# Kernel tuning notes

Measured on AMD Instinct MI355X. Metric: run time of the kernel, lower is better.

The kernel has to match this reference:

```python
import jax, jax.numpy as jnp
import numpy as np

FEATURE_SCALE = 0.25  # cfg.feature_scale
G = 4                 # deformable/offset groups
K = 3                 # deform kernel size
KK = K * K
PAD = 1


def conv2d(x, w, b=None):
    y = jax.lax.conv_general_dilated(x, w, (1, 1), ((PAD, PAD), (PAD, PAD)),
                                     dimension_numbers=('NCHW', 'OIHW', 'NCHW'))
    return y if b is None else y + b[None, :, None, None]


def bilinear_upsample_ac(x, fs):
    # F.interpolate(mode='bilinear', align_corners=True, scale_factor=fs)
    b, c, H, W = x.shape
    Ho, Wo = H * fs, W * fs
    sy = jnp.arange(Ho, dtype=x.dtype) * ((H - 1) / (Ho - 1))
    sx = jnp.arange(Wo, dtype=x.dtype) * ((W - 1) / (Wo - 1))
    y0 = jnp.clip(jnp.floor(sy).astype(jnp.int32), 0, H - 2)
    x0 = jnp.clip(jnp.floor(sx).astype(jnp.int32), 0, W - 2)
    wy = (sy - y0)[None, None, :, None]
    wx = (sx - x0)[None, None, None, :]
    rows = x[:, :, y0, :] * (1 - wy) + x[:, :, y0 + 1, :] * wy
    return rows[:, :, :, x0] * (1 - wx) + rows[:, :, :, x0 + 1] * wx


def deform_conv(x, offset, mask, w):
    # torchvision.ops.deform_conv2d, stride 1, pad 1, weight groups = 1,
    # offset/mask groups = G. offset layout: (b, G*KK*2, H, W), (dy, dx) pairs.
    b, C, H, W = x.shape
    Cg = C // G
    off = offset.reshape(b, G, KK, 2, H, W)
    ii = (jnp.arange(KK) // K).reshape(1, 1, KK, 1, 1).astype(x.dtype)
    jj = (jnp.arange(KK) % K).reshape(1, 1, KK, 1, 1).astype(x.dtype)
    ys = jnp.arange(H, dtype=x.dtype).reshape(1, 1, 1, H, 1)
    xs = jnp.arange(W, dtype=x.dtype).reshape(1, 1, 1, 1, W)
    py = ys - PAD + ii + off[:, :, :, 0]   # (b,G,KK,H,W)
    px = xs - PAD + jj + off[:, :, :, 1]
    xt = x.reshape(b, G, Cg, H, W).transpose(0, 1, 3, 4, 2)  # (b,G,H,W,Cg)
    y0f = jnp.floor(py)
    x0f = jnp.floor(px)
    wy = py - y0f
    wx = px - x0f
    y0 = y0f.astype(jnp.int32)
    x0 = x0f.astype(jnp.int32)
    bi = jnp.arange(b).reshape(b, 1, 1, 1, 1)
    gi = jnp.arange(G).reshape(1, G, 1, 1, 1)

    def corner(yi, xi, wgt):
        valid = ((yi >= 0) & (yi < H) & (xi >= 0) & (xi < W)).astype(x.dtype)
        v = xt[bi, gi, jnp.clip(yi, 0, H - 1), jnp.clip(xi, 0, W - 1)]  # (b,G,KK,H,W,Cg)
        return v * (wgt * valid)[..., None]

    s = (corner(y0, x0, (1 - wy) * (1 - wx)) + corner(y0, x0 + 1, (1 - wy) * wx)
         + corner(y0 + 1, x0, wy * (1 - wx)) + corner(y0 + 1, x0 + 1, wy * wx))
    s = s * mask.reshape(b, G, KK, H, W)[..., None]
    wr = w.reshape(w.shape[0], G, Cg, KK)
    return jnp.einsum('bgkhwc,ogck->bohw', s, wr)


def _align(sou_list, ref_list, params):
    cat_feat, offset_vs = [], []
    for i in (3, 2, 1):
        sou, ref = sou_list[i - 1], ref_list[i - 1]
        b, C, H, W = sou.shape
        Cg = C // G
        off_w, off_b, mod_w, mod_b, reg_w = params[i]
        off_in = jnp.concatenate([sou.reshape(b, G, Cg, H, W),
                                  ref.reshape(b, G, Cg, H, W)], axis=2)
        off_in = off_in.reshape(b * G, 2 * Cg, H, W)
        offset = conv2d(off_in, off_w, off_b).reshape(b, G * 2 * KK, H, W)
        rng = min(H, W) * 0.5 / 2
        offset_map = rng * 2 * jax.nn.sigmoid(offset) - rng
        modulator = 2.0 * jax.nn.sigmoid(conv2d(sou, mod_w, mod_b))
        feat = deform_conv(sou, offset_map, modulator, reg_w)
        fs = int(1 // (FEATURE_SCALE / 2 ** (i - 1)))
        oy = jnp.mean(offset_map[:, 0::2], axis=1, keepdims=True)
        ox = jnp.mean(offset_map[:, 1::2], axis=1, keepdims=True)
        ov = bilinear_upsample_ac(jnp.concatenate([oy, ox], axis=1), fs) * fs
        cat_feat.append(feat)
        offset_vs.append(ov)
    return tuple(cat_feat) + tuple(offset_vs)


def setup_inputs() -> dict:
    key = jax.random.key(0)
    ks = jax.random.split(key, 32)
    d = {}
    shapes = {1: (2, 64, 128, 128), 2: (2, 64, 64, 64), 3: (2, 64, 32, 32)}
    k = 0
    for i in (1, 2, 3):
        d[f'sou{i}'] = jax.random.normal(ks[k], shapes[i], jnp.float32); k += 1
        d[f'ref{i}'] = jax.random.normal(ks[k], shapes[i], jnp.float32); k += 1
    Cg = 64 // G
    for i in (1, 2, 3):
        d[f'off_w{i}'] = jax.random.normal(ks[k], (2 * KK, 2 * Cg, K, K), jnp.float32) * 0.05; k += 1
        d[f'off_b{i}'] = jax.random.normal(ks[k], (2 * KK,), jnp.float32) * 0.05; k += 1
        d[f'mod_w{i}'] = jax.random.normal(ks[k], (G * KK, 64, K, K), jnp.float32) * 0.05; k += 1
        d[f'mod_b{i}'] = jax.random.normal(ks[k], (G * KK,), jnp.float32) * 0.05; k += 1
        d[f'reg_w{i}'] = jax.random.normal(ks[k], (64, 64, K, K), jnp.float32) * 0.05; k += 1
    return d


def reference(sou1, sou2, sou3, ref1, ref2, ref3,
              off_w1, off_b1, mod_w1, mod_b1, reg_w1,
              off_w2, off_b2, mod_w2, mod_b2, reg_w2,
              off_w3, off_b3, mod_w3, mod_b3, reg_w3):
    params = {1: (off_w1, off_b1, mod_w1, mod_b1, reg_w1),
              2: (off_w2, off_b2, mod_w2, mod_b2, reg_w2),
              3: (off_w3, off_b3, mod_w3, mod_b3, reg_w3)}
    return _align([sou1, sou2, sou3], [ref1, ref2, ref3], params)
```

## Files before the change

### kernel.cpp

```cpp
#include <hip/hip_runtime.h>

typedef __attribute__((ext_vector_type(8))) short short8;
typedef __attribute__((ext_vector_type(4))) float f32x4;

__device__ __forceinline__ float sigmoidf_(float x) { return 1.f / (1.f + __expf(-x)); }
__device__ __forceinline__ unsigned bf16rne(float x) {
    unsigned b = __float_as_uint(x);
    return (b + 0x7FFFu + ((b >> 16) & 1u)) >> 16;
}


struct P {
    const float *sou0, *sou1, *sou2;
    const float *ref0, *ref1, *ref2;
    const float *ob0, *ob1, *ob2;
    const float *mb0, *mb1, *mb2;
    float* out;
    float* ws;
};

union U {
    uint4 u4; int4 i4; short8 s8; f32x4 f4;
};

__global__ __launch_bounds__(256) void repack_all(
    const float* __restrict__ ow0, const float* __restrict__ mw0, const float* __restrict__ rw0,
    const float* __restrict__ ow1, const float* __restrict__ mw1, const float* __restrict__ rw1,
    const float* __restrict__ ow2, const float* __restrict__ mw2, const float* __restrict__ rw2,
    float* __restrict__ dst) {
    const int lvl = blockIdx.y;
    const float* ow = lvl == 0 ? ow0 : (lvl == 1 ? ow1 : ow2);
    const float* mw = lvl == 0 ? mw0 : (lvl == 1 ? mw1 : mw2);
    const float* rw = lvl == 0 ? rw0 : (lvl == 1 ? rw1 : rw2);
    unsigned* d = (unsigned*)(dst + lvl * 62784);
    int i = blockIdx.x * 256 + threadIdx.x;
    if (i < 18432) {
        int jw = i & 3;
        int lane = (i >> 2) & 63;
        int t3 = i >> 8;
        int ks = t3 % 18, wvu = t3 / 18;
        int o = wvu * 16 + (lane & 15);
        int c0 = ks * 32 + (lane >> 4) * 8 + 2 * jw;
        int g0 = c0 / 144, r0 = c0 % 144;
        int c1 = c0 + 1;
        int g1 = c1 / 144, r1 = c1 % 144;
        float w0 = rw[o * 576 + (g0 * 16 + (r0 & 15)) * 9 + (r0 >> 4)];
        float w1 = rw[o * 576 + (g1 * 16 + (r1 & 15)) * 9 + (r1 >> 4)];
        d[i] = bf16rne(w0) | (bf16rne(w1) << 16);
    } else if (i < 23040) {
        int o2 = i - 18432;
        int jw = o2 & 3;
        int lane = (o2 >> 2) & 63;
        int t2 = o2 >> 8;
        int tap = t2 >> 1, nt = t2 & 1;
        int n = nt * 16 + (lane & 15);
        int ic0 = (lane >> 4) * 8 + 2 * jw;
        float w0 = (n < 18) ? ow[n * 288 + ic0 * 9 + tap] : 0.f;
        float w1 = (n < 18) ? ow[n * 288 + (ic0 + 1) * 9 + tap] : 0.f;
        d[36864 + o2] = bf16rne(w0) | (bf16rne(w1) << 16);
    } else if (i < 36864) {
        int o3 = i - 23040;
        int jw = o3 & 3;
        int lane = (o3 >> 2) & 63;
        int t3 = o3 >> 8;
        int nt = t3 % 3, tc = t3 / 3;
        int tap = tc >> 1, c = tc & 1;
        int n = nt * 16 + (lane & 15);
        int ic0 = c * 32 + (lane >> 4) * 8 + 2 * jw;
        float w0 = (n < 36) ? mw[n * 576 + ic0 * 9 + tap] : 0.f;
        float w1 = (n < 36) ? mw[n * 576 + (ic0 + 1) * 9 + tap] : 0.f;
        d[41472 + o3] = bf16rne(w0) | (bf16rne(w1) << 16);
    }
}

__global__ __launch_bounds__(256) void k1_prep(P p) {
    __shared__ __align__(16) char smem[28512];
    const int t = blockIdx.x;
    float* ws = p.ws;
    const int tid = threadIdx.x;

    if (t < 2688) {
        int lvl, j;
        if (t < 2048) { lvl = 0; j = t; }
        else if (t < 2560) { lvl = 1; j = t - 2048; }
        else { lvl = 2; j = t - 2560; }
        const int logW = 7 - lvl;
        const int W = 1 << logW, H = W, HW = H * W;
        const int nper = 256 >> (2 * lvl);
        const int qb = j % nper, g = (j / nper) & 3, b = j / (nper * 4);
        const int q0 = qb * 64;
        const int hlo = q0 >> logW;
        const int xlo = q0 & (W - 1);
        const int cols = (W >= 64) ? 66 : 34;
        const int rcTot = (W >= 64) ? 198 : 136;
        const float* sou = lvl == 0 ? p.sou0 : (lvl == 1 ? p.sou1 : p.sou2);
        const float* ref = lvl == 0 ? p.ref0 : (lvl == 1 ? p.ref1 : p.ref2);
        const float* bases = sou + (size_t)(b * 64 + g * 16) * HW;
        const float* baser = ref + (size_t)(b * 64 + g * 16) * HW;
        unsigned* ldsW = (unsigned*)smem;
        const bool sact = tid < rcTot;
        const int srow = tid / cols, scol = tid - srow * cols;
        const int grow = hlo - 1 + srow, gcol = xlo - 1 + scol;
        const bool inb = sact && grow >= 0 && grow < H && gcol >= 0 && gcol < W;
        const size_t goff = inb ? ((size_t)grow * W + gcol) : 0;
#pragma unroll
        for (int c8 = 0; c8 < 4; ++c8) {
            const float* p0 = (c8 < 2) ? bases + (size_t)(c8 * 8) * HW
                                       : baser + (size_t)((c8 - 2) * 8) * HW;
            float v[8];
#pragma unroll
            for (int jj = 0; jj < 8; ++jj) v[jj] = inb ? p0[(size_t)jj * HW + goff] : 0.f;
            if (sact) {
                uint4 wv;
                wv.x = bf16rne(v[0]) | (bf16rne(v[1]) << 16);
                wv.y = bf16rne(v[2]) | (bf16rne(v[3]) << 16);
                wv.z = bf16rne(v[4]) | (bf16rne(v[5]) << 16);
                wv.w = bf16rne(v[6]) | (bf16rne(v[7]) << 16);
                *(uint4*)&ldsW[tid * 20 + c8 * 4] = wv;
            }
        }
        __syncthreads();
        const int wvu = __builtin_amdgcn_readfirstlane(tid >> 6);
        const int lane = tid & 63, quad = lane >> 4, lo16 = lane & 15;
        const int qg = q0 + wvu * 16 + lo16;
        const int rowB = (qg >> logW) - hlo;
        const int colB = (qg & (W - 1)) - xlo;
        const unsigned short* ldsS = (const unsigned short*)smem;
        const unsigned* WBO = (const unsigned*)(ws + 4730880 + lvl * 62784) + 36864;
        f32x4 acc[2];
        acc[0] = (f32x4){0.f, 0.f, 0.f, 0.f};
        acc[1] = (f32x4){0.f, 0.f, 0.f, 0.f};
#pragma unroll
        for (int tap = 0; tap < 9; ++tap) {
            const int ky = tap / 3, kx = tap - ky * 3;
            const int rc = (rowB + ky) * cols + colB + kx;
            U au; au.s8 = *(const short8*)&ldsS[rc * 40 + quad * 8];
#pragma unroll
            for (int nt = 0; nt < 2; ++nt) {
                U bu; bu.u4 = *(const uint4*)(WBO + ((tap * 2 + nt) * 64 + lane) * 4);
                acc[nt] = __builtin_amdgcn_mfma_f32_16x16x32_bf16(au.s8, bu.s8, acc[nt], 0, 0, 0);
            }
        }
        const float* bias = lvl == 0 ? p.ob0 : (lvl == 1 ? p.ob1 : p.ob2);
        float* OFFM = ws + (lvl == 0 ? 0 : (lvl == 1 ? 2359296 : 2949120));
        const float rng = 0.25f * (float)H;
#pragma unroll
        for (int nt = 0; nt < 2; ++nt) {
            const int o = nt * 16 + lo16;
            if (o < 18) {
                const float bb = bias[o];
                float* op = OFFM + (size_t)(b * 72 + g * 18 + o) * HW + q0 + wvu * 16 + quad * 4;
#pragma unroll
                for (int rg = 0; rg < 4; ++rg)
                    op[rg] = rng * (2.f * sigmoidf_(acc[nt][rg] + bb) - 1.f);
            }
        }
    } else {
        const int i1 = t - 2688;
        int lvl, j;
        if (i1 < 512) { lvl = 0; j = i1; }
        else if (i1 < 640) { lvl = 1; j = i1 - 512; }
        else { lvl = 2; j = i1 - 640; }
        const int logW = 7 - lvl;
        const int W = 1 << logW, H = W, HW = H * W;
        const int nper = 256 >> (2 * lvl);
        const int qb = j % nper, b = j / nper;
        const int q0 = qb * 64;
        const int hlo = q0 >> logW;
        const int xlo = q0 & (W - 1);
        const int cols = (W >= 64) ? 66 : 34;
        const int rcTot = (W >= 64) ? 198 : 136;
        const float* sou = lvl == 0 ? p.sou0 : (lvl == 1 ? p.sou1 : p.sou2);
        const float* base = sou + (size_t)b * 64 * HW;
        unsigned* ldsW = (unsigned*)smem;
        const bool sact = tid < rcTot;
        const int srow = tid / cols, scol = tid - srow * cols;
        const int grow = hlo - 1 + srow, gcol = xlo - 1 + scol;
        const bool inb = sact && grow >= 0 && grow < H && gcol >= 0 && gcol < W;
        const size_t goff = inb ? ((size_t)grow * W + gcol) : 0;
#pragma unroll
        for (int c8 = 0; c8 < 8; ++c8) {
            const float* p0 = base + (size_t)(c8 * 8) * HW;
            float v[8];
#pragma unroll
            for (int jj = 0; jj < 8; ++jj) v[jj] = inb ? p0[(size_t)jj * HW + goff] : 0.f;
            if (sact) {
                uint4 wv;
                wv.x = bf16rne(v[0]) | (bf16rne(v[1]) << 16);
                wv.y = bf16rne(v[2]) | (bf16rne(v[3]) << 16);
                wv.z = bf16rne(v[4]) | (bf16rne(v[5]) << 16);
                wv.w = bf16rne(v[6]) | (bf16rne(v[7]) << 16);
                *(uint4*)&ldsW[tid * 36 + c8 * 4] = wv;
            }
        }
        __syncthreads();
        unsigned* XTb = (unsigned*)(ws + 4919232) +
                        (lvl == 0 ? 0 : (lvl == 1 ? 1048576 : 1310720));
#pragma unroll
        for (int u = 0; u < 2; ++u) {
            const int idx = tid * 2 + u;
            const int px = idx >> 3, gh = idx & 7;
            const int g = gh >> 1, half = gh & 1;
            const int rc = ((px >> logW) + 1) * cols + (px & (W - 1)) + 1;
            uint4 v = *(const uint4*)&ldsW[rc * 36 + g * 8 + half * 4];
            *(uint4*)(XTb + ((size_t)(b * 4 + g) * HW + q0 + px) * 8 + half * 4) = v;
        }
        const int wvu = __builtin_amdgcn_readfirstlane(tid >> 6);
        const int lane = tid & 63, quad = lane >> 4, lo16 = lane & 15;
        const int qg = q0 + wvu * 16 + lo16;
        const int rowB = (qg >> logW) - hlo;
        const int colB = (qg & (W - 1)) - xlo;
        const unsigned short* ldsS = (const unsigned short*)smem;
        const unsigned* WBM = (const unsigned*)(ws + 4730880 + lvl * 62784) + 41472;
        f32x4 acc[3];
        acc[0] = (f32x4){0.f, 0.f, 0.f, 0.f};
        acc[1] = (f32x4){0.f, 0.f, 0.f, 0.f};
        acc[2] = (f32x4){0.f, 0.f, 0.f, 0.f};
#pragma unroll
        for (int tap = 0; tap < 9; ++tap) {
            const int ky = tap / 3, kx = tap - ky * 3;
            const int rc = (rowB + ky) * cols + colB + kx;
#pragma unroll
            for (int c = 0; c < 2; ++c) {
                U au; au.s8 = *(const short8*)&ldsS[rc * 72 + c * 32 + quad * 8];
#pragma unroll
                for (int nt = 0; nt < 3; ++nt) {
                    U bu;
                    bu.u4 = *(const uint4*)(WBM + (((tap * 2 + c) * 3 + nt) * 64 + lane) * 4);
                    acc[nt] = __builtin_amdgcn_mfma_f32_16x16x32_bf16(au.s8, bu.s8, acc[nt], 0, 0, 0);
                }
            }
        }
        const float* bias = lvl == 0 ? p.mb0 : (lvl == 1 ? p.mb1 : p.mb2);
        float* MOD = ws + (lvl == 0 ? 3096576 : (lvl == 1 ? 4276224 : 4571136));
#pragma unroll
        for (int nt = 0; nt < 3; ++nt) {
            const int o = nt * 16 + lo16;
            if (o < 36) {
                const float bb = bias[o];
                float* op = MOD + (size_t)(b * 36 + o) * HW + q0 + wvu * 16 + quad * 4;
#pragma unroll
                for (int rg = 0; rg < 4; ++rg)
                    op[rg] = 2.f * sigmoidf_(acc[nt][rg] + bb);
            }
        }
    }
}

__global__ __launch_bounds__(256) void k2_fused(P p) {
    __shared__ unsigned lds[96 * 33];
    const int t = blockIdx.x;
    float* ws = p.ws;
    const int tid = threadIdx.x;
    if (t < 1344) {
        int lvl, j;
        if (t < 1024) { lvl = 0; j = t; }
        else if (t < 1280) { lvl = 1; j = t - 1024; }
        else { lvl = 2; j = t - 1280; }
        const int logW = 7 - lvl;
        const int W = 1 << logW, H = W, HW = H * W;
        const int nper = 512 >> (2 * lvl);
        const int qb = j % nper, b = j / nper;
        const int q0 = qb * 32;
        const float* OFFM = ws + (lvl == 0 ? 0 : (lvl == 1 ? 2359296 : 2949120));
        const float* MOD = ws + (lvl == 0 ? 3096576 : (lvl == 1 ? 4276224 : 4571136));
        const unsigned* XTb = (const unsigned*)(ws + 4919232) +
                              (lvl == 0 ? 0 : (lvl == 1 ? 1048576 : 1310720));
        const unsigned* WB = (const unsigned*)(ws + 4730880 + lvl * 62784);
        float* outp = p.out + (lvl == 0 ? 655360 : (lvl == 1 ? 131072 : 0));
        const int wvu = __builtin_amdgcn_readfirstlane(tid >> 6);
        const int lane = tid & 63, quad = lane >> 4, lo16 = lane & 15;
        f32x4 acc[2];
        acc[0] = (f32x4){0.f, 0.f, 0.f, 0.f};
        acc[1] = (f32x4){0.f, 0.f, 0.f, 0.f};
        for (int c = 0; c < 3; ++c) {
            if (c) __syncthreads();
#pragma unroll
            for (int it = 0; it < 2; ++it) {
                const int task = it * 256 + tid;
                if (task < 384) {
                    const int gkl = task >> 5, px = task & 31;
                    const int gk = c * 12 + gkl;
                    const int g = gk / 9, k = gk - g * 9;
                    const int q = q0 + px;
                    const int h = q >> logW, xp = q & (W - 1);
                    const int ky = k / 3, kx = k - ky * 3;
                    float dy = OFFM[(size_t)(b * 72 + g * 18 + 2 * k) * HW + q];
                    float dx = OFFM[(size_t)(b * 72 + g * 18 + 2 * k + 1) * HW + q];
                    float m = MOD[(size_t)(b * 36 + g * 9 + k) * HW + q];
                    float py = (float)(h - 1 + ky) + dy;
                    float pxx = (float)(xp - 1 + kx) + dx;
                    float y0f = floorf(py), x0f = floorf(pxx);
                    float wy = py - y0f, wx = pxx - x0f;
                    int y0 = (int)y0f, x0 = (int)x0f;
                    const unsigned* xg = XTb + (size_t)(b * 4 + g) * HW * 8;
                    float s[16];
#pragma unroll
                    for (int cc = 0; cc < 16; ++cc) s[cc] = 0.f;
#pragma unroll
                    for (int cor = 0; cor < 4; ++cor) {
                        int yy = y0 + (cor >> 1), xx = x0 + (cor & 1);
                        float cw = ((cor >> 1) ? wy : 1.f - wy) * ((cor & 1) ? wx : 1.f - wx);
                        cw = (yy >= 0 && yy < H && xx >= 0 && xx < W) ? cw * m : 0.f;
                        int yc = min(max(yy, 0), H - 1), xc = min(max(xx, 0), W - 1);
                        const uint4* cp = (const uint4*)(xg + (size_t)((yc << logW) + xc) * 8);
                        unsigned cbuf[8];
                        *(uint4*)&cbuf[0] = cp[0];
                        *(uint4*)&cbuf[4] = cp[1];
#pragma unroll
                        for (int pr = 0; pr < 8; ++pr) {
                            float lo = __uint_as_float(cbuf[pr] << 16);
                            float hi = __uint_as_float(cbuf[pr] & 0xFFFF0000u);
                            s[2 * pr] = fmaf(cw, lo, s[2 * pr]);
                            s[2 * pr + 1] = fmaf(cw, hi, s[2 * pr + 1]);
                        }
                    }
#pragma unroll
                    for (int pr = 0; pr < 8; ++pr)
                        lds[(gkl * 8 + pr) * 33 + px] =
                            bf16rne(s[2 * pr]) | (bf16rne(s[2 * pr + 1]) << 16);
                }
            }
            __syncthreads();
            uint4 bfr[6];
#pragma unroll
            for (int k6 = 0; k6 < 6; ++k6)
                bfr[k6] = *(const uint4*)(WB + (((wvu * 18 + c * 6 + k6) * 64 + lane) << 2));
#pragma unroll
            for (int k6 = 0; k6 < 6; ++k6) {
                const int rb = k6 * 16 + quad * 4;
                U bu; bu.u4 = bfr[k6];
#pragma unroll
                for (int mt = 0; mt < 2; ++mt) {
                    const int px = mt * 16 + lo16;
                    U au;
                    au.i4.x = (int)lds[(rb + 0) * 33 + px];
                    au.i4.y = (int)lds[(rb + 1) * 33 + px];
                    au.i4.z = (int)lds[(rb + 2) * 33 + px];
                    au.i4.w = (int)lds[(rb + 3) * 33 + px];
                    acc[mt] = __builtin_amdgcn_mfma_f32_16x16x32_bf16(au.s8, bu.s8, acc[mt], 0, 0, 0);
                }
            }
        }
        float* op = outp + (size_t)(b * 64 + wvu * 16 + lo16) * HW + q0;
#pragma unroll
        for (int mt = 0; mt < 2; ++mt)
#pragma unroll
            for (int rg = 0; rg < 4; ++rg)
                op[mt * 16 + quad * 4 + rg] = acc[mt][rg];
    } else {
        int i = t - 1344;
        int lvl, j;
        if (i < 128) { lvl = 0; j = i; }
        else if (i < 160) { lvl = 1; j = i - 128; }
        else { lvl = 2; j = i - 160; }
        const int HW = 16384 >> (2 * lvl);
        const int nper = 64 >> (2 * lvl);
        const int qb = j % nper, b = j / nper;
        const float* OFFM = ws + (lvl == 0 ? 0 : (lvl == 1 ? 2359296 : 2949120));
        float* MEAN = ws + (lvl == 0 ? 4644864 : (lvl == 1 ? 4710400 : 4726784));
        const int q = qb * 256 + tid;
        const float* pp = OFFM + (size_t)b * 72 * HW + q;
        float sy = 0.f, sx = 0.f;
#pragma unroll
        for (int u = 0; u < 36; ++u) {
            sy += pp[(size_t)(2 * u) * HW];
            sx += pp[(size_t)(2 * u + 1) * HW];
        }
        MEAN[(size_t)(b * 2) * HW + q] = sy * (1.f / 36.f);
        MEAN[(size_t)(b * 2 + 1) * HW + q] = sx * (1.f / 36.f);
    }
}

__global__ __launch_bounds__(256) void k3_up(P p) {
    float* ws = p.ws;
    int flat = ((int)blockIdx.x * 256 + (int)threadIdx.x) * 4;
    int lvl = flat >> 20;
    int r = flat & 1048575;
    int b = r >> 19, c = (r >> 18) & 1;
    int pix = r & 262143;
    int yo = pix >> 9, xo = pix & 511;
    const int H = 128 >> lvl, W = H;
    const float* MEAN = ws + (lvl == 0 ? 4644864 : (lvl == 1 ? 4710400 : 4726784));
    const float* m = MEAN + (size_t)(b * 2 + c) * H * W;
    float* o = p.out + (lvl == 0 ? 4849664 : (lvl == 1 ? 3801088 : 2752512)) +
               ((size_t)(b * 2 + c) * 512 + yo) * 512 + xo;
    const float fs = (float)(4 << lvl);
    const float sc = (float)(H - 1) * (1.f / 511.f);
    float sy = yo * sc;
    int y0 = min((int)sy, H - 2);
    float wy = sy - (float)y0;
    float rr[4];
#pragma unroll
    for (int u = 0; u < 4; ++u) {
        float sx = (float)(xo + u) * sc;
        int x0 = min((int)sx, W - 2);
        float wx = sx - (float)x0;
        float v00 = m[y0 * W + x0], v01 = m[y0 * W + x0 + 1];
        float v10 = m[(y0 + 1) * W + x0], v11 = m[(y0 + 1) * W + x0 + 1];
        float r0 = v00 * (1.f - wy) + v10 * wy;
        float r1 = v01 * (1.f - wy) + v11 * wy;
        rr[u] = (r0 * (1.f - wx) + r1 * wx) * fs;
    }
    *(float4*)o = make_float4(rr[0], rr[1], rr[2], rr[3]);
}

extern "C" void kernel_launch(void* const* d_in, const int* in_sizes, int n_in,
                              void* d_out, int out_size, void* d_ws, size_t ws_size,
                              hipStream_t stream) {
    const float* fin[21];
    for (int i = 0; i < 21; ++i) fin[i] = (const float*)d_in[i];
    P p;
    if (in_sizes[1] == in_sizes[0]) {
        p.sou0 = fin[0]; p.ref0 = fin[1];
        p.sou1 = fin[2]; p.ref1 = fin[3];
        p.sou2 = fin[4]; p.ref2 = fin[5];
    } else {
        p.sou0 = fin[0]; p.sou1 = fin[1]; p.sou2 = fin[2];
        p.ref0 = fin[3]; p.ref1 = fin[4]; p.ref2 = fin[5];
    }
    p.ob0 = fin[7]; p.mb0 = fin[9];
    p.ob1 = fin[12]; p.mb1 = fin[14];
    p.ob2 = fin[17]; p.mb2 = fin[19];
    p.out = (float*)d_out;
    p.ws = (float*)d_ws;

    repack_all<<<dim3(144, 3), 256, 0, stream>>>(
        fin[6], fin[8], fin[10], fin[11], fin[13], fin[15], fin[16], fin[18], fin[20],
        p.ws + 4730880);
    k1_prep<<<dim3(3360), 256, 0, stream>>>(p);
    k2_fused<<<dim3(1512), 256, 0, stream>>>(p);
    k3_up<<<dim3(3072), 256, 0, stream>>>(p);
}
```

Measured before the change: 185.0 us.

## Merge offset and modulation conv blocks so one block loads each source tile once

Merges the separate offset-conv blocks (one per group) and modulation-conv blocks into a single block per spatial tile. The block stages all 64 source channels in LDS once and runs both convolutions from it, then reloads the reference channels into the same buffer. The offset conv's K dimension is repacked to tap-major 16-channel chunks (5 k-steps, zero-padded) so it can use the 72-wide LDS layout. This cuts repeated global reads of the sou/ref inputs and the grid from 3360 to 672 blocks. In exchange each block holds more accumulators and does longer serial work, and the padded K adds some wasted MFMA work.

After: 180.3 us. 2.5% less time.

```diff
diff --git a/kernel.cpp b/kernel.cpp
--- a/kernel.cpp
+++ b/kernel.cpp
@@ -47,19 +47,23 @@
         float w0 = rw[o * 576 + (g0 * 16 + (r0 & 15)) * 9 + (r0 >> 4)];
         float w1 = rw[o * 576 + (g1 * 16 + (r1 & 15)) * 9 + (r1 >> 4)];
         d[i] = bf16rne(w0) | (bf16rne(w1) << 16);
-    } else if (i < 23040) {
+    } else if (i < 23552) {
         int o2 = i - 18432;
         int jw = o2 & 3;
         int lane = (o2 >> 2) & 63;
         int t2 = o2 >> 8;
-        int tap = t2 >> 1, nt = t2 & 1;
+        int nt = t2 & 1;
+        int hk = t2 >> 1;
+        int ks = hk % 5, h = hk / 5;
         int n = nt * 16 + (lane & 15);
-        int ic0 = (lane >> 4) * 8 + 2 * jw;
-        float w0 = (n < 18) ? ow[n * 288 + ic0 * 9 + tap] : 0.f;
-        float w1 = (n < 18) ? ow[n * 288 + (ic0 + 1) * 9 + tap] : 0.f;
+        int K = ks * 32 + (lane >> 4) * 8 + 2 * jw;
+        int tap = K >> 4, ch = K & 15;
+        bool ok = (n < 18) && (tap < 9);
+        float w0 = ok ? ow[n * 288 + (h * 16 + ch) * 9 + tap] : 0.f;
+        float w1 = ok ? ow[n * 288 + (h * 16 + ch + 1) * 9 + tap] : 0.f;
         d[36864 + o2] = bf16rne(w0) | (bf16rne(w1) << 16);
-    } else if (i < 36864) {
-        int o3 = i - 23040;
+    } else if (i < 37376) {
+        int o3 = i - 23552;
         int jw = o3 & 3;
         int lane = (o3 >> 2) & 63;
         int t3 = o3 >> 8;
@@ -69,7 +73,7 @@
         int ic0 = c * 32 + (lane >> 4) * 8 + 2 * jw;
         float w0 = (n < 36) ? mw[n * 576 + ic0 * 9 + tap] : 0.f;
         float w1 = (n < 36) ? mw[n * 576 + (ic0 + 1) * 9 + tap] : 0.f;
-        d[41472 + o3] = bf16rne(w0) | (bf16rne(w1) << 16);
+        d[41984 + o3] = bf16rne(w0) | (bf16rne(w1) << 16);
     }
 }
 
@@ -79,158 +83,151 @@
     float* ws = p.ws;
     const int tid = threadIdx.x;
 
-    if (t < 2688) {
-        int lvl, j;
-        if (t < 2048) { lvl = 0; j = t; }
-        else if (t < 2560) { lvl = 1; j = t - 2048; }
-        else { lvl = 2; j = t - 2560; }
-        const int logW = 7 - lvl;
-        const int W = 1 << logW, H = W, HW = H * W;
-        const int nper = 256 >> (2 * lvl);
-        const int qb = j % nper, g = (j / nper) & 3, b = j / (nper * 4);
-        const int q0 = qb * 64;
-        const int hlo = q0 >> logW;
-        const int xlo = q0 & (W - 1);
-        const int cols = (W >= 64) ? 66 : 34;
-        const int rcTot = (W >= 64) ? 198 : 136;
-        const float* sou = lvl == 0 ? p.sou0 : (lvl == 1 ? p.sou1 : p.sou2);
-        const float* ref = lvl == 0 ? p.ref0 : (lvl == 1 ? p.ref1 : p.ref2);
-        const float* bases = sou + (size_t)(b * 64 + g * 16) * HW;
-        const float* baser = ref + (size_t)(b * 64 + g * 16) * HW;
-        unsigned* ldsW = (unsigned*)smem;
-        const bool sact = tid < rcTot;
-        const int srow = tid / cols, scol = tid - srow * cols;
-        const int grow = hlo - 1 + srow, gcol = xlo - 1 + scol;
-        const bool inb = sact && grow >= 0 && grow < H && gcol >= 0 && gcol < W;
-        const size_t goff = inb ? ((size_t)grow * W + gcol) : 0;
-#pragma unroll
-        for (int c8 = 0; c8 < 4; ++c8) {
-            const float* p0 = (c8 < 2) ? bases + (size_t)(c8 * 8) * HW
-                                       : baser + (size_t)((c8 - 2) * 8) * HW;
-            float v[8];
-#pragma unroll
-            for (int jj = 0; jj < 8; ++jj) v[jj] = inb ? p0[(size_t)jj * HW + goff] : 0.f;
-            if (sact) {
-                uint4 wv;
-                wv.x = bf16rne(v[0]) | (bf16rne(v[1]) << 16);
-                wv.y = bf16rne(v[2]) | (bf16rne(v[3]) << 16);
-                wv.z = bf16rne(v[4]) | (bf16rne(v[5]) << 16);
-                wv.w = bf16rne(v[6]) | (bf16rne(v[7]) << 16);
-                *(uint4*)&ldsW[tid * 20 + c8 * 4] = wv;
-            }
-        }
-        __syncthreads();
-        const int wvu = __builtin_amdgcn_readfirstlane(tid >> 6);
-        const int lane = tid & 63, quad = lane >> 4, lo16 = lane & 15;
-        const int qg = q0 + wvu * 16 + lo16;
-        const int rowB = (qg >> logW) - hlo;
-        const int colB = (qg & (W - 1)) - xlo;
-        const unsigned short* ldsS = (const unsigned short*)smem;
-        const unsigned* WBO = (const unsigned*)(ws + 4730880 + lvl * 62784) + 36864;
-        f32x4 acc[2];
-        acc[0] = (f32x4){0.f, 0.f, 0.f, 0.f};
-        acc[1] = (f32x4){0.f, 0.f, 0.f, 0.f};
-#pragma unroll
-        for (int tap = 0; tap < 9; ++tap) {
-            const int ky = tap / 3, kx = tap - ky * 3;
-            const int rc = (rowB + ky) * cols + colB + kx;
-            U au; au.s8 = *(const short8*)&ldsS[rc * 40 + quad * 8];
+    int lvl, j;
+    if (t < 512) { lvl = 0; j = t; }
+    else if (t < 640) { lvl = 1; j = t - 512; }
+    else { lvl = 2; j = t - 640; }
+    const int logW = 7 - lvl;
+    const int W = 1 << logW, H = W, HW = H * W;
+    const int nper = 256 >> (2 * lvl);
+    const int qb = j % nper, b = j / nper;
+    const int q0 = qb * 64;
+    const int hlo = q0 >> logW;
+    const int xlo = q0 & (W - 1);
+    const int cols = (W >= 64) ? 66 : 34;
+    const int rcTot = (W >= 64) ? 198 : 136;
+    const float* sou = lvl == 0 ? p.sou0 : (lvl == 1 ? p.sou1 : p.sou2);
+    const float* ref = lvl == 0 ? p.ref0 : (lvl == 1 ? p.ref1 : p.ref2);
+    const float* base_s = sou + (size_t)b * 64 * HW;
+    const float* base_r = ref + (size_t)b * 64 * HW;
+    unsigned* ldsW = (unsigned*)smem;
+    const bool sact = tid < rcTot;
+    const int srow = tid / cols, scol = tid - srow * cols;
+    const int grow = hlo - 1 + srow, gcol = xlo - 1 + scol;
+    const bool inb = sact && grow >= 0 && grow < H && gcol >= 0 && gcol < W;
+    const size_t goff = inb ? ((size_t)grow * W + gcol) : 0;
+
+#pragma unroll
+    for (int c8 = 0; c8 < 8; ++c8) {
+        const float* p0 = base_s + (size_t)(c8 * 8) * HW;
+        float v[8];
+#pragma unroll
+        for (int jj = 0; jj < 8; ++jj) v[jj] = inb ? p0[(size_t)jj * HW + goff] : 0.f;
+        if (sact) {
+            uint4 wv;
+            wv.x = bf16rne(v[0]) | (bf16rne(v[1]) << 16);
+            wv.y = bf16rne(v[2]) | (bf16rne(v[3]) << 16);
+            wv.z = bf16rne(v[4]) | (bf16rne(v[5]) << 16);
+            wv.w = bf16rne(v[6]) | (bf16rne(v[7]) << 16);
+            *(uint4*)&ldsW[tid * 36 + c8 * 4] = wv;
+        }
+    }
+    __syncthreads();
+
+    unsigned* XTb = (unsigned*)(ws + 4919232) +
+                    (lvl == 0 ? 0 : (lvl == 1 ? 1048576 : 1310720));
+#pragma unroll
+    for (int u = 0; u < 2; ++u) {
+        const int idx = tid * 2 + u;
+        const int px = idx >> 3, gh = idx & 7;
+        const int g = gh >> 1, half = gh & 1;
+        const int rc = ((px >> logW) + 1) * cols + (px & (W - 1)) + 1;
+        uint4 v = *(const uint4*)&ldsW[rc * 36 + g * 8 + half * 4];
+        *(uint4*)(XTb + ((size_t)(b * 4 + g) * HW + q0 + px) * 8 + half * 4) = v;
+    }
+
+    const int wvu = __builtin_amdgcn_readfirstlane(tid >> 6);
+    const int lane = tid & 63, quad = lane >> 4, lo16 = lane & 15;
+    const int qg = q0 + wvu * 16 + lo16;
+    const int rowB = (qg >> logW) - hlo;
+    const int colB = (qg & (W - 1)) - xlo;
+    const unsigned short* ldsS = (const unsigned short*)smem;
+    const unsigned* WREPu = (const unsigned*)(ws + 4730880 + lvl * 62784);
+    const unsigned* WBO2 = WREPu + 36864;
+    const unsigned* WBM = WREPu + 41984;
+
+    f32x4 accM[3], accO[4][2];
+#pragma unroll
+    for (int nt = 0; nt < 3; ++nt) accM[nt] = (f32x4){0.f, 0.f, 0.f, 0.f};
+#pragma unroll
+    for (int g = 0; g < 4; ++g)
+#pragma unroll
+        for (int nt = 0; nt < 2; ++nt) accO[g][nt] = (f32x4){0.f, 0.f, 0.f, 0.f};
+
+#pragma unroll
+    for (int tap = 0; tap < 9; ++tap) {
+        const int ky = tap / 3, kx = tap - ky * 3;
+        const int rc = (rowB + ky) * cols + colB + kx;
+#pragma unroll
+        for (int c = 0; c < 2; ++c) {
+            U au; au.s8 = *(const short8*)&ldsS[rc * 72 + c * 32 + quad * 8];
+#pragma unroll
+            for (int nt = 0; nt < 3; ++nt) {
+                U bu;
+                bu.u4 = *(const uint4*)(WBM + (((tap * 2 + c) * 3 + nt) * 64 + lane) * 4);
+                accM[nt] = __builtin_amdgcn_mfma_f32_16x16x32_bf16(au.s8, bu.s8, accM[nt], 0, 0, 0);
+            }
+        }
+    }
+#pragma unroll
+    for (int ks = 0; ks < 5; ++ks) {
+        const int Kbase = ks * 32 + quad * 8;
+        const int tap = min(Kbase >> 4, 8);
+        const int ky = tap / 3, kx = tap - ky * 3;
+        const int rc = (rowB + ky) * cols + colB + kx;
+        const int choff = Kbase & 15;
+#pragma unroll
+        for (int g = 0; g < 4; ++g) {
+            U au; au.s8 = *(const short8*)&ldsS[rc * 72 + g * 16 + choff];
 #pragma unroll
             for (int nt = 0; nt < 2; ++nt) {
-                U bu; bu.u4 = *(const uint4*)(WBO + ((tap * 2 + nt) * 64 + lane) * 4);
-                acc[nt] = __builtin_amdgcn_mfma_f32_16x16x32_bf16(au.s8, bu.s8, acc[nt], 0, 0, 0);
-            }
-        }
-        const float* bias = lvl == 0 ? p.ob0 : (lvl == 1 ? p.ob1 : p.ob2);
-        float* OFFM = ws + (lvl == 0 ? 0 : (lvl == 1 ? 2359296 : 2949120));
-        const float rng = 0.25f * (float)H;
-#pragma unroll
-        for (int nt = 0; nt < 2; ++nt) {
-            const int o = nt * 16 + lo16;
-            if (o < 18) {
-                const float bb = bias[o];
-                float* op = OFFM + (size_t)(b * 72 + g * 18 + o) * HW + q0 + wvu * 16 + quad * 4;
-#pragma unroll
-                for (int rg = 0; rg < 4; ++rg)
-                    op[rg] = rng * (2.f * sigmoidf_(acc[nt][rg] + bb) - 1.f);
-            }
-        }
-    } else {
-        const int i1 = t - 2688;
-        int lvl, j;
-        if (i1 < 512) { lvl = 0; j = i1; }
-        else if (i1 < 640) { lvl = 1; j = i1 - 512; }
-        else { lvl = 2; j = i1 - 640; }
-        const int logW = 7 - lvl;
-        const int W = 1 << logW, H = W, HW = H * W;
-        const int nper = 256 >> (2 * lvl);
-        const int qb = j % nper, b = j / nper;
-        const int q0 = qb * 64;
-        const int hlo = q0 >> logW;
-        const int xlo = q0 & (W - 1);
-        const int cols = (W >= 64) ? 66 : 34;
-        const int rcTot = (W >= 64) ? 198 : 136;
-        const float* sou = lvl == 0 ? p.sou0 : (lvl == 1 ? p.sou1 : p.sou2);
-        const float* base = sou + (size_t)b * 64 * HW;
-        unsigned* ldsW = (unsigned*)smem;
-        const bool sact = tid < rcTot;
-        const int srow = tid / cols, scol = tid - srow * cols;
-        const int grow = hlo - 1 + srow, gcol = xlo - 1 + scol;
-        const bool inb = sact && grow >= 0 && grow < H && gcol >= 0 && gcol < W;
-        const size_t goff = inb ? ((size_t)grow * W + gcol) : 0;
-#pragma unroll
-        for (int c8 = 0; c8 < 8; ++c8) {
-            const float* p0 = base + (size_t)(c8 * 8) * HW;
-            float v[8];
-#pragma unroll
-            for (int jj = 0; jj < 8; ++jj) v[jj] = inb ? p0[(size_t)jj * HW + goff] : 0.f;
-            if (sact) {
-                uint4 wv;
-                wv.x = bf16rne(v[0]) | (bf16rne(v[1]) << 16);
-                wv.y = bf16rne(v[2]) | (bf16rne(v[3]) << 16);
-                wv.z = bf16rne(v[4]) | (bf16rne(v[5]) << 16);
-                wv.w = bf16rne(v[6]) | (bf16rne(v[7]) << 16);
-                *(uint4*)&ldsW[tid * 36 + c8 * 4] = wv;
-            }
-        }
-        __syncthreads();
-        unsigned* XTb = (unsigned*)(ws + 4919232) +
-                        (lvl == 0 ? 0 : (lvl == 1 ? 1048576 : 1310720));
-#pragma unroll
-        for (int u = 0; u < 2; ++u) {
-            const int idx = tid * 2 + u;
-            const int px = idx >> 3, gh = idx & 7;
-            const int g = gh >> 1, half = gh & 1;
-            const int rc = ((px >> logW) + 1) * cols + (px & (W - 1)) + 1;
-            uint4 v = *(const uint4*)&ldsW[rc * 36 + g * 8 + half * 4];
-            *(uint4*)(XTb + ((size_t)(b * 4 + g) * HW + q0 + px) * 8 + half * 4) = v;
-        }
-        const int wvu = __builtin_amdgcn_readfirstlane(tid >> 6);
-        const int lane = tid & 63, quad = lane >> 4, lo16 = lane & 15;
-        const int qg = q0 + wvu * 16 + lo16;
-        const int rowB = (qg >> logW) - hlo;
-        const int colB = (qg & (W - 1)) - xlo;
-        const unsigned short* ldsS = (const unsigned short*)smem;
-        const unsigned* WBM = (const unsigned*)(ws + 4730880 + lvl * 62784) + 41472;
-        f32x4 acc[3];
-        acc[0] = (f32x4){0.f, 0.f, 0.f, 0.f};
-        acc[1] = (f32x4){0.f, 0.f, 0.f, 0.f};
-        acc[2] = (f32x4){0.f, 0.f, 0.f, 0.f};
-#pragma unroll
-        for (int tap = 0; tap < 9; ++tap) {
-            const int ky = tap / 3, kx = tap - ky * 3;
-            const int rc = (rowB + ky) * cols + colB + kx;
-#pragma unroll
-            for (int c = 0; c < 2; ++c) {
-                U au; au.s8 = *(const short8*)&ldsS[rc * 72 + c * 32 + quad * 8];
-#pragma unroll
-                for (int nt = 0; nt < 3; ++nt) {
-                    U bu;
-                    bu.u4 = *(const uint4*)(WBM + (((tap * 2 + c) * 3 + nt) * 64 + lane) * 4);
-                    acc[nt] = __builtin_amdgcn_mfma_f32_16x16x32_bf16(au.s8, bu.s8, acc[nt], 0, 0, 0);
-                }
-            }
-        }
+                U bu;
+                bu.u4 = *(const uint4*)(WBO2 + ((ks * 2 + nt) * 64 + lane) * 4);
+                accO[g][nt] =
+                    __builtin_amdgcn_mfma_f32_16x16x32_bf16(au.s8, bu.s8, accO[g][nt], 0, 0, 0);
+            }
+        }
+    }
+    __syncthreads();
+
+#pragma unroll
+    for (int c8 = 0; c8 < 8; ++c8) {
+        const float* p0 = base_r + (size_t)(c8 * 8) * HW;
+        float v[8];
+#pragma unroll
+        for (int jj = 0; jj < 8; ++jj) v[jj] = inb ? p0[(size_t)jj * HW + goff] : 0.f;
+        if (sact) {
+            uint4 wv;
+            wv.x = bf16rne(v[0]) | (bf16rne(v[1]) << 16);
+            wv.y = bf16rne(v[2]) | (bf16rne(v[3]) << 16);
+            wv.z = bf16rne(v[4]) | (bf16rne(v[5]) << 16);
+            wv.w = bf16rne(v[6]) | (bf16rne(v[7]) << 16);
+            *(uint4*)&ldsW[tid * 36 + c8 * 4] = wv;
+        }
+    }
+    __syncthreads();
+
+#pragma unroll
+    for (int ks = 0; ks < 5; ++ks) {
+        const int Kbase = ks * 32 + quad * 8;
+        const int tap = min(Kbase >> 4, 8);
+        const int ky = tap / 3, kx = tap - ky * 3;
+        const int rc = (rowB + ky) * cols + colB + kx;
+        const int choff = Kbase & 15;
+#pragma unroll
+        for (int g = 0; g < 4; ++g) {
+            U au; au.s8 = *(const short8*)&ldsS[rc * 72 + g * 16 + choff];
+#pragma unroll
+            for (int nt = 0; nt < 2; ++nt) {
+                U bu;
+                bu.u4 = *(const uint4*)(WBO2 + (((5 + ks) * 2 + nt) * 64 + lane) * 4);
+                accO[g][nt] =
+                    __builtin_amdgcn_mfma_f32_16x16x32_bf16(au.s8, bu.s8, accO[g][nt], 0, 0, 0);
+            }
+        }
+    }
+
+    {
         const float* bias = lvl == 0 ? p.mb0 : (lvl == 1 ? p.mb1 : p.mb2);
         float* MOD = ws + (lvl == 0 ? 3096576 : (lvl == 1 ? 4276224 : 4571136));
 #pragma unroll
@@ -241,9 +238,27 @@
                 float* op = MOD + (size_t)(b * 36 + o) * HW + q0 + wvu * 16 + quad * 4;
 #pragma unroll
                 for (int rg = 0; rg < 4; ++rg)
-                    op[rg] = 2.f * sigmoidf_(acc[nt][rg] + bb);
-            }
-        }
+                    op[rg] = 2.f * sigmoidf_(accM[nt][rg] + bb);
+            }
+        }
+    }
+    {
+        const float* bias = lvl == 0 ? p.ob0 : (lvl == 1 ? p.ob1 : p.ob2);
+        float* OFFM = ws + (lvl == 0 ? 0 : (lvl == 1 ? 2359296 : 2949120));
+        const float rng = 0.25f * (float)H;
+#pragma unroll
+        for (int g = 0; g < 4; ++g)
+#pragma unroll
+            for (int nt = 0; nt < 2; ++nt) {
+                const int o = nt * 16 + lo16;
+                if (o < 18) {
+                    const float bb = bias[o];
+                    float* op = OFFM + (size_t)(b * 72 + g * 18 + o) * HW + q0 + wvu * 16 + quad * 4;
+#pragma unroll
+                    for (int rg = 0; rg < 4; ++rg)
+                        op[rg] = rng * (2.f * sigmoidf_(accO[g][nt][rg] + bb) - 1.f);
+                }
+            }
     }
 }
 
@@ -425,10 +440,10 @@
     p.out = (float*)d_out;
     p.ws = (float*)d_ws;
 
-    repack_all<<<dim3(144, 3), 256, 0, stream>>>(
+    repack_all<<<dim3(146, 3), 256, 0, stream>>>(
         fin[6], fin[8], fin[10], fin[11], fin[13], fin[15], fin[16], fin[18], fin[20],
         p.ws + 4730880);
-    k1_prep<<<dim3(3360), 256, 0, stream>>>(p);
+    k1_prep<<<dim3(672), 256, 0, stream>>>(p);
     k2_fused<<<dim3(1512), 256, 0, stream>>>(p);
     k3_up<<<dim3(3072), 256, 0, stream>>>(p);
 }
```
